# Performance work log

Measured on AMD Instinct MI355X. Metric: run time of the kernel, lower is better.

## Reference

```python
import jax, jax.numpy as jnp
import numpy as np

HEAD_SIZE = 64

def setup_inputs() -> dict:
    key = jax.random.key(0)
    k1, k2, k3, k4 = jax.random.split(key, 4)
    B, T, C, H = 8, 2048, 1024, HEAD_SIZE
    x = jax.random.normal(k1, (B, T, C), dtype=jnp.float32)
    attention_mask = jnp.ones((B, T), dtype=jnp.int32)
    # nn.Linear(C, H, bias=False): store as [C, H] so y = x @ W
    s = 1.0 / np.sqrt(C)
    Wk = jax.random.normal(k2, (C, H), dtype=jnp.float32) * s
    Wq = jax.random.normal(k3, (C, H), dtype=jnp.float32) * s
    Wv = jax.random.normal(k4, (C, H), dtype=jnp.float32) * s
    return {"x": x, "attention_mask": attention_mask, "Wk": Wk, "Wq": Wq, "Wv": Wv}

def reference(x, attention_mask, Wk, Wq, Wv):
    # x: [B, T, C]; projections -> [B, T, H]
    k = jnp.einsum('btc,ch->bth', x, Wk)
    q = jnp.einsum('btc,ch->bth', x, Wq)
    v = jnp.einsum('btc,ch->bth', x, Wv)
    scale = k.shape[-1] ** -0.5
    wei = jnp.einsum('bqh,bkh->bqk', q, k) * scale  # [B, T, T]
    mask = attention_mask[:, None, :]               # [B, 1, T] key-padding mask
    wei = jnp.where(mask == 0, -jnp.inf, wei)
    wei_soft = jax.nn.softmax(wei, axis=-1)
    # dropout p=0.0 (eval mode): identity
    out = jnp.einsum('bqk,bkh->bqh', wei_soft, v)   # [B, T, H]
    return out
```

## Files before the change

### kernel.cpp

```cpp
#include <hip/hip_runtime.h>
#include <hip/hip_bf16.h>

typedef __bf16 bf16;
typedef __bf16 bf16x4 __attribute__((ext_vector_type(4)));
typedef __bf16 bf16x8 __attribute__((ext_vector_type(8)));
typedef float f32x4 __attribute__((ext_vector_type(4)));

#define NB 8
#define NT 2048
#define NC 1024
#define NH 64

#define QSCALE 0.18033688011112042f

__device__ inline f32x4 zero4() {
    f32x4 z; z[0] = 0.f; z[1] = 0.f; z[2] = 0.f; z[3] = 0.f; return z;
}

__device__ inline float fast_exp2(float x) {
    float r;
    asm volatile("v_exp_f32 %0, %1" : "=v"(r) : "v"(x));
    return r;
}

__global__ __launch_bounds__(256) void pack_w(const float* __restrict__ Wq,
                                              const float* __restrict__ Wk,
                                              const float* __restrict__ Wv,
                                              bf16* __restrict__ Wt2) {
    const int g = blockIdx.x * 256 + threadIdx.x;
    const int l = g & 63;
    const int kc = (g >> 6) & 1;
    const int kt = (g >> 7) & 15;
    const int nf = g >> 11;
    const int n = nf * 16 + (l & 15);
    const int k0 = kt * 64 + kc * 32 + (l >> 4) * 8;
    const float* W = (n < 64) ? Wq : (n < 128) ? Wk : Wv;
    const float sc = (n < 64) ? QSCALE : 1.0f;
    const int h = n & 63;
    bf16x8 o;
#pragma unroll
    for (int e = 0; e < 8; ++e) o[e] = (bf16)(W[(k0 + e) * NH + h] * sc);
    *reinterpret_cast<bf16x8*>(Wt2 + (size_t)g * 8) = o;
}

__global__ __launch_bounds__(256, 2) void qkv_gemm(const float* __restrict__ x,
                                                   const bf16* __restrict__ Wt2,
                                                   bf16* __restrict__ qp,
                                                   bf16* __restrict__ kp2,
                                                   bf16* __restrict__ vt2) {
    __shared__ bf16 xs[2][64][72];
    const int tid = threadIdx.x;
    const int wave = tid >> 6, lane = tid & 63;
    const int l16 = lane & 15, lhi = lane >> 4;
    const int qh = wave & 1;
    const int ch = wave >> 1;
    const int row0 = blockIdx.x * 64;
    const bf16* wb = Wt2 + (size_t)ch * 98304 + lane * 8;

    f32x4 acc[2][6];
#pragma unroll
    for (int mr = 0; mr < 2; ++mr)
#pragma unroll
        for (int nf = 0; nf < 6; ++nf) acc[mr][nf] = zero4();

    const int sr = tid >> 4;
    const int sc = (tid & 15) * 4;

    float4 xv[3][4];
    bf16x8 bfr[2][12];

#define LOAD_X(SLOT, KT)  do { \
    _Pragma("unroll") for (int _i = 0; _i < 4; ++_i) \
        xv[SLOT][_i] = *reinterpret_cast<const float4*>( \
            &x[(size_t)(row0 + sr + _i * 16) * NC + (KT) * 64 + sc]); \
} while (0)

#define LOAD_B(SLOT, KT)  do { \
    _Pragma("unroll") for (int _nf = 0; _nf < 6; ++_nf) \
        _Pragma("unroll") for (int _kc = 0; _kc < 2; ++_kc) \
            bfr[SLOT][_nf * 2 + _kc] = *reinterpret_cast<const bf16x8*>( \
                wb + _nf * 16384 + (KT) * 1024 + _kc * 512); \
} while (0)

#define WRITE_XS(BUF, SLOT)  do { \
    _Pragma("unroll") for (int _i = 0; _i < 4; ++_i) { \
        bf16x4 _w; \
        _w[0] = (bf16)xv[SLOT][_i].x; _w[1] = (bf16)xv[SLOT][_i].y; \
        _w[2] = (bf16)xv[SLOT][_i].z; _w[3] = (bf16)xv[SLOT][_i].w; \
        *reinterpret_cast<bf16x4*>(&xs[BUF][sr + _i * 16][sc]) = _w; \
    } \
} while (0)

    LOAD_X(0, 0);
    LOAD_X(1, 1);
    LOAD_X(2, 2);
    LOAD_B(0, 0);
    WRITE_XS(0, 0);
    __syncthreads();

#pragma unroll
    for (int kt = 0; kt < 16; ++kt) {
        const int cur = kt & 1, nxt = cur ^ 1;
        if (kt < 13) LOAD_X(kt % 3, kt + 3);
        bf16x8 a[2][2];
#pragma unroll
        for (int mr = 0; mr < 2; ++mr)
#pragma unroll
            for (int kc = 0; kc < 2; ++kc)
                a[mr][kc] = *reinterpret_cast<const bf16x8*>(
                    &xs[cur][qh * 32 + mr * 16 + l16][kc * 32 + lhi * 8]);
        if (kt < 15) WRITE_XS(nxt, (kt + 1) % 3);
        if (kt < 15) LOAD_B(nxt, kt + 1);
        __syncthreads();
        __builtin_amdgcn_s_setprio(1);
#pragma unroll
        for (int nf = 0; nf < 6; ++nf)
#pragma unroll
            for (int kc = 0; kc < 2; ++kc)
#pragma unroll
                for (int mr = 0; mr < 2; ++mr)
                    acc[mr][nf] = __builtin_amdgcn_mfma_f32_16x16x32_bf16(
                        a[mr][kc], bfr[cur][nf * 2 + kc], acc[mr][nf], 0, 0, 0);
        __builtin_amdgcn_s_setprio(0);
    }
#undef LOAD_X
#undef LOAD_B
#undef WRITE_XS

#pragma unroll
    for (int mr = 0; mr < 2; ++mr)
#pragma unroll
    for (int nf = 0; nf < 6; ++nf) {
        const int col = ch * 96 + nf * 16 + l16;
#pragma unroll
        for (int r = 0; r < 4; ++r) {
            const int row = row0 + qh * 32 + mr * 16 + lhi * 4 + r;
            const bf16 val = (bf16)acc[mr][nf][r];
            const int bb = row >> 11, kv = row & (NT - 1);
            const int t = kv >> 6;
            if (col < 64) {
                qp[(size_t)row * NH + col] = val;
            } else if (col < 128) {
                const int h = col - 64;
                const int kvb = (kv >> 4) & 3;
                const int lK = ((h & 31) >> 3) * 16 + (kv & 15);
                kp2[((((size_t)(bb * 32 + t) * 4 + kvb) * 2 + (h >> 5)) * 64 + lK) * 8 + (h & 7)] = val;
            } else {
                const int h = col - 128;
                const int kcV = (kv >> 5) & 1;
                const int lV = ((kv & 31) >> 3) * 16 + (h & 15);
                vt2[((((size_t)(bb * 32 + t) * 2 + kcV) * 4 + (h >> 4)) * 64 + lV) * 8 + (kv & 7)] = val;
            }
        }
    }
}

__global__ __launch_bounds__(256, 2) void attn(const bf16* __restrict__ qp,
                                               const bf16* __restrict__ kp2,
                                               const bf16* __restrict__ vt2,
                                               const int* __restrict__ mask,
                                               float* __restrict__ out) {
    __shared__ __align__(16) char smem[4 * 2 * 16 * 68 * 4];
    bf16 (*p_lds)[64][20] = reinterpret_cast<bf16 (*)[64][20]>(smem);
    float (*sm_o)[2][16][68] = reinterpret_cast<float (*)[2][16][68]>(smem);
    __shared__ float sm_m[4][2][16], sm_l[4][2][16];

    const int tid = threadIdx.x;
    const int sp = tid >> 6, lane = tid & 63;
    const int l16 = lane & 15, lhi = lane >> 4;
    const int b = blockIdx.y;
    const int q_base = blockIdx.x * 32;
    const int tb = sp * 8;
    bf16* const pw = &p_lds[sp][0][0];

    bf16x8 aq[2][2];
#pragma unroll
    for (int t = 0; t < 2; ++t)
#pragma unroll
        for (int hc = 0; hc < 2; ++hc)
            aq[t][hc] = *reinterpret_cast<const bf16x8*>(
                &qp[((size_t)b * NT + q_base + t * 16 + l16) * NH + hc * 32 + lhi * 8]);

    const bf16* kw = kp2 + (size_t)b * 131072 + (size_t)tb * 4096 + lane * 8;
    const bf16* vw = vt2 + (size_t)b * 131072 + (size_t)tb * 4096 + lane * 8;
    const int*  mw = mask + b * NT + tb * 64 + lhi * 4;

    float m[2] = {-1e30f, -1e30f}, l[2] = {0.f, 0.f};
    f32x4 o[2][4];
#pragma unroll
    for (int t = 0; t < 2; ++t)
#pragma unroll
        for (int hb = 0; hb < 4; ++hb) o[t][hb] = zero4();

#pragma unroll
    for (int it = 0; it < 8; ++it) {
        const int fo = it * 4096;
        bf16x8 kf[8];
#pragma unroll
        for (int i = 0; i < 8; ++i)
            kf[i] = *reinterpret_cast<const bf16x8*>(kw + fo + i * 512);
        int4 mv[4];
#pragma unroll
        for (int kvb = 0; kvb < 4; ++kvb)
            mv[kvb] = *reinterpret_cast<const int4*>(mw + it * 64 + kvb * 16);
        f32x4 s[2][4];
        __builtin_amdgcn_s_setprio(1);
#pragma unroll
        for (int t = 0; t < 2; ++t)
#pragma unroll
            for (int kvb = 0; kvb < 4; ++kvb) {
                s[t][kvb] = zero4();
                s[t][kvb] = __builtin_amdgcn_mfma_f32_16x16x32_bf16(kf[kvb * 2], aq[t][0], s[t][kvb], 0, 0, 0);
                s[t][kvb] = __builtin_amdgcn_mfma_f32_16x16x32_bf16(kf[kvb * 2 + 1], aq[t][1], s[t][kvb], 0, 0, 0);
            }
        __builtin_amdgcn_s_setprio(0);
        bf16x8 vf[8];
#pragma unroll
        for (int i = 0; i < 8; ++i)
            vf[i] = *reinterpret_cast<const bf16x8*>(vw + fo + i * 512);
        f32x4 biasv[4];
#pragma unroll
        for (int kvb = 0; kvb < 4; ++kvb) {
            biasv[kvb][0] = mv[kvb].x ? 0.f : -1e30f;
            biasv[kvb][1] = mv[kvb].y ? 0.f : -1e30f;
            biasv[kvb][2] = mv[kvb].z ? 0.f : -1e30f;
            biasv[kvb][3] = mv[kvb].w ? 0.f : -1e30f;
        }
#pragma unroll
        for (int t = 0; t < 2; ++t) {
#pragma unroll
            for (int kvb = 0; kvb < 4; ++kvb) s[t][kvb] += biasv[kvb];
            float tm = s[t][0][0];
#pragma unroll
            for (int kvb = 0; kvb < 4; ++kvb)
#pragma unroll
                for (int r = 0; r < 4; ++r) tm = fmaxf(tm, s[t][kvb][r]);
            tm = fmaxf(tm, __shfl_xor(tm, 16));
            tm = fmaxf(tm, __shfl_xor(tm, 32));
            if (!__all(tm <= m[t] + 8.f)) {
                const float mn = fmaxf(m[t], tm);
                const float alpha = fast_exp2(m[t] - mn);
                m[t] = mn;
                l[t] *= alpha;
                float ar[4];
#pragma unroll
                for (int r = 0; r < 4; ++r) ar[r] = __shfl(alpha, lhi * 4 + r);
#pragma unroll
                for (int hb = 0; hb < 4; ++hb)
#pragma unroll
                    for (int r = 0; r < 4; ++r) o[t][hb][r] *= ar[r];
            }
            float ps = 0.f;
#pragma unroll
            for (int kvb = 0; kvb < 4; ++kvb)
#pragma unroll
                for (int r = 0; r < 4; ++r) {
                    const float p = fast_exp2(s[t][kvb][r] - m[t]);
                    s[t][kvb][r] = p;
                    ps += p;
                }
            ps += __shfl_xor(ps, 16);
            ps += __shfl_xor(ps, 32);
            l[t] += ps;
#pragma unroll
            for (int kvb = 0; kvb < 4; ++kvb) {
                bf16x4 w;
                w[0] = (bf16)s[t][kvb][0]; w[1] = (bf16)s[t][kvb][1];
                w[2] = (bf16)s[t][kvb][2]; w[3] = (bf16)s[t][kvb][3];
                const int row = l16 + 16 * ((kvb * 2 + (lhi >> 1)) & 3);
                *reinterpret_cast<bf16x4*>(pw + row * 20 + (kvb >> 1) * 8 + (lhi & 1) * 4) = w;
            }
            __builtin_amdgcn_s_setprio(1);
#pragma unroll
            for (int kc = 0; kc < 2; ++kc) {
                const bf16* pr = pw + lane * 20 + kc * 8;
                const bf16x4 lo = *reinterpret_cast<const bf16x4*>(pr);
                const bf16x4 hi = *reinterpret_cast<const bf16x4*>(pr + 4);
                const bf16x8 pa = __builtin_shufflevector(lo, hi, 0, 1, 2, 3, 4, 5, 6, 7);
#pragma unroll
                for (int hb = 0; hb < 4; ++hb)
                    o[t][hb] = __builtin_amdgcn_mfma_f32_16x16x32_bf16(pa, vf[kc * 4 + hb], o[t][hb], 0, 0, 0);
            }
            __builtin_amdgcn_s_setprio(0);
        }
    }

    __syncthreads();
#pragma unroll
    for (int t = 0; t < 2; ++t) {
#pragma unroll
        for (int hb = 0; hb < 4; ++hb)
#pragma unroll
            for (int r = 0; r < 4; ++r)
                sm_o[sp][t][lhi * 4 + r][hb * 16 + l16] = o[t][hb][r];
        if (lhi == 0) {
            sm_m[sp][t][l16] = m[t];
            sm_l[sp][t][l16] = l[t];
        }
    }
    __syncthreads();

#pragma unroll
    for (int e = 0; e < 8; ++e) {
        const int idx = e * 256 + tid;
        const int row = idx >> 6;
        const int col = idx & 63;
        const int t2 = row >> 4, r16 = row & 15;
        float M = sm_m[0][t2][r16];
#pragma unroll
        for (int s2 = 1; s2 < 4; ++s2) M = fmaxf(M, sm_m[s2][t2][r16]);
        float L = 0.f, accv = 0.f;
#pragma unroll
        for (int s2 = 0; s2 < 4; ++s2) {
            const float w = fast_exp2(sm_m[s2][t2][r16] - M);
            L += w * sm_l[s2][t2][r16];
            accv += w * sm_o[s2][t2][r16][col];
        }
        out[((size_t)b * NT + q_base + row) * NH + col] = accv / L;
    }
}

extern "C" void kernel_launch(void* const* d_in, const int* in_sizes, int n_in,
                              void* d_out, int out_size, void* d_ws, size_t ws_size,
                              hipStream_t stream) {
    const float* x    = (const float*)d_in[0];
    const int*   mask = (const int*)d_in[1];
    const float* Wk   = (const float*)d_in[2];
    const float* Wq   = (const float*)d_in[3];
    const float* Wv   = (const float*)d_in[4];
    float* out = (float*)d_out;

    char* ws = (char*)d_ws;
    bf16* Wt2 = (bf16*)(ws);
    bf16* qp  = (bf16*)(ws + (512 << 10));
    bf16* kp2 = (bf16*)(ws + (512 << 10) + (2 << 20));
    bf16* vt2 = (bf16*)(ws + (512 << 10) + (4 << 20));

    pack_w<<<dim3(96), dim3(256), 0, stream>>>(Wq, Wk, Wv, Wt2);
    qkv_gemm<<<dim3(256), dim3(256), 0, stream>>>(x, Wt2, qp, kp2, vt2);
    attn<<<dim3(64, 8), dim3(256), 0, stream>>>(qp, kp2, vt2, mask, out);
}
```

Measured before the change: 48.51 us.

## Use 512-thread attention blocks covering 64 queries and skip mask bias when unmasked

The attention kernel now launches 512-thread blocks, with eight waves split into two query groups of 32 rows. Each group keeps the four-way KV split, so a block covers 64 queries and the grid halves. This is meant to reduce per-block overhead and allow sharing through cache, but it doubles LDS use per block and may hurt occupancy or wave scheduling. The change also adds a wave-uniform check that skips building and adding the mask bias when every key in the tile is unmasked.

```diff
diff --git a/kernel.cpp b/kernel.cpp
--- a/kernel.cpp
+++ b/kernel.cpp
@@ -155,23 +155,26 @@
     }
 }
 
-__global__ __launch_bounds__(256, 2) void attn(const bf16* __restrict__ qp,
+__global__ __launch_bounds__(512, 2) void attn(const bf16* __restrict__ qp,
                                                const bf16* __restrict__ kp2,
                                                const bf16* __restrict__ vt2,
                                                const int* __restrict__ mask,
                                                float* __restrict__ out) {
-    __shared__ __align__(16) char smem[4 * 2 * 16 * 68 * 4];
+    __shared__ __align__(16) char smem[4 * 64 * 68 * 4];
     bf16 (*p_lds)[64][20] = reinterpret_cast<bf16 (*)[64][20]>(smem);
-    float (*sm_o)[2][16][68] = reinterpret_cast<float (*)[2][16][68]>(smem);
-    __shared__ float sm_m[4][2][16], sm_l[4][2][16];
+    float (*sm_o)[64][68] = reinterpret_cast<float (*)[64][68]>(smem);
+    __shared__ float sm_m[4][64], sm_l[4][64];
 
     const int tid = threadIdx.x;
-    const int sp = tid >> 6, lane = tid & 63;
+    const int wave = tid >> 6, lane = tid & 63;
     const int l16 = lane & 15, lhi = lane >> 4;
+    const int sp = wave & 3;
+    const int qg = wave >> 2;
     const int b = blockIdx.y;
-    const int q_base = blockIdx.x * 32;
+    const int q_blk = blockIdx.x * 64;
+    const int q_base = q_blk + qg * 32;
     const int tb = sp * 8;
-    bf16* const pw = &p_lds[sp][0][0];
+    bf16* const pw = &p_lds[wave][0][0];
 
     bf16x8 aq[2][2];
 #pragma unroll
@@ -218,18 +221,27 @@
 #pragma unroll
         for (int i = 0; i < 8; ++i)
             vf[i] = *reinterpret_cast<const bf16x8*>(vw + fo + i * 512);
+        const int okm = (mv[0].x != 0) & (mv[0].y != 0) & (mv[0].z != 0) & (mv[0].w != 0) &
+                        (mv[1].x != 0) & (mv[1].y != 0) & (mv[1].z != 0) & (mv[1].w != 0) &
+                        (mv[2].x != 0) & (mv[2].y != 0) & (mv[2].z != 0) & (mv[2].w != 0) &
+                        (mv[3].x != 0) & (mv[3].y != 0) & (mv[3].z != 0) & (mv[3].w != 0);
+        const bool allone = __all(okm);
         f32x4 biasv[4];
-#pragma unroll
-        for (int kvb = 0; kvb < 4; ++kvb) {
-            biasv[kvb][0] = mv[kvb].x ? 0.f : -1e30f;
-            biasv[kvb][1] = mv[kvb].y ? 0.f : -1e30f;
-            biasv[kvb][2] = mv[kvb].z ? 0.f : -1e30f;
-            biasv[kvb][3] = mv[kvb].w ? 0.f : -1e30f;
+        if (!allone) {
+#pragma unroll
+            for (int kvb = 0; kvb < 4; ++kvb) {
+                biasv[kvb][0] = mv[kvb].x ? 0.f : -1e30f;
+                biasv[kvb][1] = mv[kvb].y ? 0.f : -1e30f;
+                biasv[kvb][2] = mv[kvb].z ? 0.f : -1e30f;
+                biasv[kvb][3] = mv[kvb].w ? 0.f : -1e30f;
+            }
         }
 #pragma unroll
         for (int t = 0; t < 2; ++t) {
-#pragma unroll
-            for (int kvb = 0; kvb < 4; ++kvb) s[t][kvb] += biasv[kvb];
+            if (!allone) {
+#pragma unroll
+                for (int kvb = 0; kvb < 4; ++kvb) s[t][kvb] += biasv[kvb];
+            }
             float tm = s[t][0][0];
 #pragma unroll
             for (int kvb = 0; kvb < 4; ++kvb)
@@ -288,35 +300,35 @@
     __syncthreads();
 #pragma unroll
     for (int t = 0; t < 2; ++t) {
+        const int rbase = qg * 32 + t * 16;
 #pragma unroll
         for (int hb = 0; hb < 4; ++hb)
 #pragma unroll
             for (int r = 0; r < 4; ++r)
-                sm_o[sp][t][lhi * 4 + r][hb * 16 + l16] = o[t][hb][r];
+                sm_o[sp][rbase + lhi * 4 + r][hb * 16 + l16] = o[t][hb][r];
         if (lhi == 0) {
-            sm_m[sp][t][l16] = m[t];
-            sm_l[sp][t][l16] = l[t];
+            sm_m[sp][rbase + l16] = m[t];
+            sm_l[sp][rbase + l16] = l[t];
         }
     }
     __syncthreads();
 
 #pragma unroll
     for (int e = 0; e < 8; ++e) {
-        const int idx = e * 256 + tid;
+        const int idx = e * 512 + tid;
         const int row = idx >> 6;
         const int col = idx & 63;
-        const int t2 = row >> 4, r16 = row & 15;
-        float M = sm_m[0][t2][r16];
-#pragma unroll
-        for (int s2 = 1; s2 < 4; ++s2) M = fmaxf(M, sm_m[s2][t2][r16]);
+        float M = sm_m[0][row];
+#pragma unroll
+        for (int s2 = 1; s2 < 4; ++s2) M = fmaxf(M, sm_m[s2][row]);
         float L = 0.f, accv = 0.f;
 #pragma unroll
         for (int s2 = 0; s2 < 4; ++s2) {
-            const float w = fast_exp2(sm_m[s2][t2][r16] - M);
-            L += w * sm_l[s2][t2][r16];
-            accv += w * sm_o[s2][t2][r16][col];
-        }
-        out[((size_t)b * NT + q_base + row) * NH + col] = accv / L;
+            const float w = fast_exp2(sm_m[s2][row] - M);
+            L += w * sm_l[s2][row];
+            accv += w * sm_o[s2][row][col];
+        }
+        out[((size_t)b * NT + q_blk + row) * NH + col] = accv / L;
     }
 }
 
@@ -338,5 +350,5 @@
 
     pack_w<<<dim3(96), dim3(256), 0, stream>>>(Wq, Wk, Wv, Wt2);
     qkv_gemm<<<dim3(256), dim3(256), 0, stream>>>(x, Wt2, qp, kp2, vt2);
-    attn<<<dim3(64, 8), dim3(256), 0, stream>>>(qp, kp2, vt2, mask, out);
-}
+    attn<<<dim3(32, 8), dim3(512), 0, stream>>>(qp, kp2, vt2, mask, out);
+}
```

Result: faster. 47.07 us (-3.0%).
